# Performance work log

Measured on AMD Instinct MI355X. Metric: run time of the kernel, lower is better.

The kernel has to match this reference:

```python
import jax, jax.numpy as jnp
import numpy as np

HID = 128
EMB = 100

def _sru(x, W, b):
    # x: [B,L,D]; W: [D,3H]; b: [2H]. SRU (Lei et al.):
    #   u = [x_tilde, f_pre, r_pre]; c_t = f_t*c_{t-1} + (1-f_t)*x_tilde; h_t = r_t*tanh(c_t)
    u = jnp.einsum('bld,dk->blk', x, W)            # [B,L,3H]
    xt, fp, rp = jnp.split(u, 3, axis=-1)
    bf, br = jnp.split(b, 2)
    f = jax.nn.sigmoid(fp + bf)
    r = jax.nn.sigmoid(rp + br)
    g = (1.0 - f) * xt
    def comb(e1, e2):
        a1, b1 = e1
        a2, b2 = e2
        return a1 * a2, a2 * b1 + b2
    _, c = jax.lax.associative_scan(comb, (f, g), axis=1)  # parallel linear scan
    h = r * jnp.tanh(c)                             # [B,L,H]
    return h, c[:, -1]

def _conv_relu_gmax(x, w, bias, pad):
    # x: [B,256,1,1]; w: [16,256,k,k]; global max pool (interprets MaxPool2d(max_len) as global)
    y = jax.lax.conv_general_dilated(x, w, (1, 1), [(pad, pad), (pad, pad)],
                                     dimension_numbers=('NCHW', 'OIHW', 'NCHW'))
    y = jax.nn.relu(y + bias[None, :, None, None])
    return jnp.max(y, axis=(2, 3))                  # [B,16]

def setup_inputs() -> dict:
    key = jax.random.key(0)
    ks = jax.random.split(key, 12)
    B, L, V, NC = 8, 20000, 50000, 10
    index = jax.random.randint(ks[0], (B, L), 0, V, dtype=jnp.int64)
    emb = jax.random.normal(ks[1], (V, EMB), jnp.float32) * 0.1
    sru_W = jax.random.normal(ks[2], (EMB, 3 * HID), jnp.float32) / np.sqrt(EMB)
    sru_b = jnp.zeros((2 * HID,), jnp.float32)
    w1 = jax.random.normal(ks[3], (16, 2 * HID, 5, 5), jnp.float32) / np.sqrt(2 * HID * 25)
    b1 = jnp.zeros((16,), jnp.float32)
    w2 = jax.random.normal(ks[4], (16, 2 * HID, 4, 4), jnp.float32) / np.sqrt(2 * HID * 16)
    b2 = jnp.zeros((16,), jnp.float32)
    w3 = jax.random.normal(ks[5], (16, 2 * HID, 3, 3), jnp.float32) / np.sqrt(2 * HID * 9)
    b3 = jnp.zeros((16,), jnp.float32)
    out_W = jax.random.normal(ks[6], (48, NC), jnp.float32) / np.sqrt(48)
    out_b = jnp.zeros((NC,), jnp.float32)
    return {"index": index, "emb": emb, "sru_W": sru_W, "sru_b": sru_b,
            "w1": w1, "b1": b1, "w2": w2, "b2": b2, "w3": w3, "b3": b3,
            "out_W": out_W, "out_b": out_b}

def reference(index, emb, sru_W, sru_b, w1, b1, w2, b2, w3, b3, out_W, out_b):
    B, L = index.shape
    # Faithful reproduction of the aliased in-place reversal: y = index, then
    # y[row][j] = index[L-1-j] mutates the shared buffer, yielding
    # mutated[j] = orig[L-1-j] for j <= (L-1)//2 else orig[j]; BOTH branches
    # then embed this same mutated tensor (x aliases index in the original).
    j = jnp.arange(L)
    mutated = jnp.where((2 * j)[None, :] <= (L - 1), index[:, L - 1 - j], index)
    x = emb[mutated]                                # [B,L,100]
    h, _ = _sru(x, sru_W, sru_b)                    # both SRU passes see identical input
    hcat = jnp.concatenate([h, h], axis=2)          # [B,L,256]
    pooled = jnp.mean(hcat, axis=1)                 # AvgPool1d(kernel=L) -> [B,256]
    xc = pooled[:, :, None, None]                   # [B,256,1,1]
    f1 = _conv_relu_gmax(xc, w1, b1, 2)
    f2 = _conv_relu_gmax(xc, w2, b2, 2)
    f3 = _conv_relu_gmax(xc, w3, b3, 2)
    feats = jnp.concatenate([f1, f2, f3], axis=1)   # [B,48]
    return feats @ out_W + out_b                    # 'pred' logits [B,n_class]
```

## Files before the change

kernel.cpp:

```cpp
#include <hip/hip_runtime.h>
#include <math.h>

#define EMBD 100
#define HIDN 128
#define LSEQ 20000
#define TCS  128
#define WUP  32
#define NCH  ((LSEQ + TCS - 1) / TCS)

typedef __attribute__((ext_vector_type(8))) short bf16x8;
typedef __attribute__((ext_vector_type(4))) float f32x4;
typedef unsigned int u32;

__device__ __forceinline__ u32 f2bf_rne(float x) {
    u32 u = __float_as_uint(x);
    return (u + 0x7FFFu + ((u >> 16) & 1u)) >> 16;
}
__device__ __forceinline__ float bf2f(u32 b) { return __uint_as_float(b << 16); }

__device__ __forceinline__ float sigmoid_fast(float x) {
    float e = __expf(-x);
    return __builtin_amdgcn_rcpf(1.f + e);
}
__device__ __forceinline__ float tanh_fast(float x) {
    float e = __expf(2.f * x);
    return 1.f - 2.f * __builtin_amdgcn_rcpf(e + 1.f);
}

__global__ __launch_bounds__(256) void k_prep(const float* __restrict__ W,
                                              short* __restrict__ Wpk,
                                              const float* __restrict__ w1,
                                              const float* __restrict__ w2,
                                              const float* __restrict__ w3,
                                              float* __restrict__ Wc)
{
    const int blk = blockIdx.x;
    if (blk < 192) {
        int t = blk * 256 + threadIdx.x;
        int k = t / 384, c = t - k * 384;
        float w = (k < EMBD) ? W[k * 384 + c] : 0.0f;
        int kt = k >> 5, ct = c >> 4;
        int cg = ct & 7, c3 = ct >> 3;
        int l  = ((k >> 3) & 3) * 16 + (c & 15);
        int j  = k & 7;
        Wpk[(size_t)cg * 6144 + kt * 1536 + c3 * 512 + l * 8 + j] = (short)f2bf_rne(w);
    } else {
        int t = (blk - 192) * 256 + threadIdx.x;
        if (t >= 14 * 16 * HIDN) return;
        int k = t & 127, d = t >> 7;
        int o = d & 15, tap = d >> 4;
        const float* w; int KH, ki, kj;
        if (tap == 0)      { w = w1; KH = 5; ki = 2; kj = 2; }
        else if (tap < 5)  { w = w2; KH = 4; int p = tap - 1; ki = 1 + (p >> 1); kj = 1 + (p & 1); }
        else               { w = w3; KH = 3; int p = tap - 5; ki = p / 3; kj = p % 3; }
        float v = w[((size_t)(o * 256 + k) * KH + ki) * KH + kj]
                + w[((size_t)(o * 256 + k + 128) * KH + ki) * KH + kj];
        Wc[(size_t)d * HIDN + k] = v;
    }
}

__global__ __launch_bounds__(256) void k_build(const float* __restrict__ emb,
                                               const short* __restrict__ Wpk,
                                               const float* __restrict__ bias,
                                               u32* __restrict__ FGR, int V)
{
    const int lane = threadIdx.x & 63;
    const int wave = threadIdx.x >> 6;
    const int v0   = blockIdx.x * 128 + wave * 32;
    const int arow = lane & 15;
    const int kgrp = lane >> 4;

    bf16x8 Ah[2][4];
#pragma unroll
    for (int s = 0; s < 2; s++) {
        int va = v0 + s * 16 + arow; if (va > V - 1) va = V - 1;
        const float* erow = emb + (size_t)va * EMBD;
#pragma unroll
        for (int kt = 0; kt < 4; kt++) {
            int kbase = kt * 32 + kgrp * 8;
#pragma unroll
            for (int j = 0; j < 8; j++) {
                int k = kbase + j;
                Ah[s][kt][j] = (short)((k < EMBD) ? f2bf_rne(erow[k]) : 0);
            }
        }
    }

#pragma unroll 1
    for (int cgp = 0; cgp < 4; cgp++) {
        f32x4 acc[2][2][3];
#pragma unroll
        for (int s = 0; s < 2; s++)
#pragma unroll
            for (int h = 0; h < 2; h++)
#pragma unroll
                for (int c3 = 0; c3 < 3; c3++)
                    acc[s][h][c3] = f32x4{0.f, 0.f, 0.f, 0.f};

#pragma unroll
        for (int kt = 0; kt < 4; kt++) {
            const short* pL = Wpk + (size_t)cgp * 6144 + kt * 1536 + lane * 8;
            const short* pH = pL + 4 * 6144;
#pragma unroll
            for (int c3 = 0; c3 < 3; c3++) {
                bf16x8 BL = *reinterpret_cast<const bf16x8*>(pL + c3 * 512);
                bf16x8 BH = *reinterpret_cast<const bf16x8*>(pH + c3 * 512);
#pragma unroll
                for (int s = 0; s < 2; s++) {
                    acc[s][0][c3] = __builtin_amdgcn_mfma_f32_16x16x32_bf16(Ah[s][kt], BL, acc[s][0][c3], 0, 0, 0);
                    acc[s][1][c3] = __builtin_amdgcn_mfma_f32_16x16x32_bf16(Ah[s][kt], BH, acc[s][1][c3], 0, 0, 0);
                }
            }
        }

        const int kl = cgp * 16 + arow;
        const float bfL = bias[kl],      brL = bias[128 + kl];
        const float bfH = bias[kl + 64], brH = bias[192 + kl];
#pragma unroll
        for (int s = 0; s < 2; s++) {
#pragma unroll
            for (int reg = 0; reg < 4; reg++) {
                int v = v0 + s * 16 + kgrp * 4 + reg;
                if (v < V) {
                    float fL = sigmoid_fast(acc[s][0][1][reg] + bfL);
                    float rL = sigmoid_fast(acc[s][0][2][reg] + brL);
                    float gL = (1.f - fL) * acc[s][0][0][reg];
                    float fH = sigmoid_fast(acc[s][1][1][reg] + bfH);
                    float rH = sigmoid_fast(acc[s][1][2][reg] + brH);
                    float gH = (1.f - fH) * acc[s][1][0][reg];
                    u32 d0 = f2bf_rne(fL) | (f2bf_rne(gL) << 16);
                    u32 d1 = f2bf_rne(fH) | (f2bf_rne(gH) << 16);
                    u32 d2 = f2bf_rne(rL) | (f2bf_rne(rH) << 16);
                    *reinterpret_cast<uint2*>(FGR + (size_t)v * 192 + kl * 2) = make_uint2(d0, d1);
                    FGR[(size_t)v * 192 + 128 + kl] = d2;
                }
            }
        }
    }
}

__device__ __forceinline__ int mut_src(int t) {
    return (2 * t <= LSEQ - 1) ? (LSEQ - 1 - t) : t;
}

#define LOADB(Abuf, Rbuf, BT, NEEDR)                                       \
    { const int* sp = svp + (BT) * 8;                                      \
      _Pragma("unroll")                                                    \
      for (int i = 0; i < 8; i++) {                                        \
          int v = sp[i];                                                   \
          Abuf[i] = fgp[(size_t)v * 96 + lane];                            \
          Rbuf[i] = (NEEDR) ? FGR[(size_t)v * 192 + 128 + lane] : 0u;      \
      } }

#define STEP8(Abuf, Rbuf, DO_H)                                            \
    _Pragma("unroll")                                                      \
    for (int i = 0; i < 8; i++) {                                          \
        uint2 w = Abuf[i];                                                 \
        c0 = fmaf(__uint_as_float(w.x << 16), c0, __uint_as_float(w.x & 0xFFFF0000u)); \
        c1 = fmaf(__uint_as_float(w.y << 16), c1, __uint_as_float(w.y & 0xFFFF0000u)); \
        if (DO_H) {                                                        \
            u32 rr = Rbuf[i];                                              \
            h0 = fmaf(__uint_as_float(rr << 16),         tanh_fast(c0), h0); \
            h1 = fmaf(__uint_as_float(rr & 0xFFFF0000u), tanh_fast(c1), h1); \
        } }

__global__ __launch_bounds__(256) void k_scan(const int* __restrict__ idx,
                                              const u32* __restrict__ FGR,
                                              float* __restrict__ hpart)
{
    const int wave = threadIdx.x >> 6, lane = threadIdx.x & 63;
    const int ch = blockIdx.x * 4 + wave, b = blockIdx.y;
    if (ch >= NCH) return;
    const int t0 = ch * TCS;
    const int tw = (t0 >= WUP) ? (t0 - WUP) : 0;
    const int tend = (t0 + TCS < LSEQ) ? (t0 + TCS) : LSEQ;
    const int nsteps = tend - tw;
    const int nb = nsteps >> 3;
    const int wb = (t0 - tw) >> 3;
    __shared__ int sv[4][TCS + WUP];
    int* svp = sv[wave];
    for (int s = lane; s < nsteps; s += 64)
        svp[s] = idx[b * LSEQ + mut_src(tw + s)];

    const uint2* fgp = reinterpret_cast<const uint2*>(FGR);
    float c0 = 0.f, c1 = 0.f, h0 = 0.f, h1 = 0.f;
    uint2 A0[8], A1[8], A2[8]; u32 R0[8], R1[8], R2[8];

    LOADB(A0, R0, 0, 0 >= wb);
    LOADB(A1, R1, 1, 1 >= wb);

    for (int bt = 0; bt < nb; bt++) {
        if (bt + 2 < nb) { LOADB(A2, R2, bt + 2, bt + 2 >= wb); }
        if (bt >= wb) { STEP8(A0, R0, true); }
        else          { STEP8(A0, R0, false); }
#pragma unroll
        for (int i = 0; i < 8; i++) {
            A0[i] = A1[i]; R0[i] = R1[i];
            A1[i] = A2[i]; R1[i] = R2[i];
        }
    }

    float* hp = hpart + (size_t)(b * NCH + ch) * HIDN;
    hp[lane]      = h0;
    hp[lane + 64] = h1;
}

__global__ __launch_bounds__(1024) void k_head(const float* __restrict__ hpart,
                                               const float* __restrict__ Wc,
                                               const float* __restrict__ b1,
                                               const float* __restrict__ b2,
                                               const float* __restrict__ b3,
                                               const float* __restrict__ oW,
                                               const float* __restrict__ ob,
                                               float* __restrict__ out)
{
    __shared__ float red[8][HIDN];
    __shared__ float m[HIDN];
    __shared__ float dots[224];
    __shared__ float feats[48];
    const int b = blockIdx.x, tid = threadIdx.x;

    {
        int k = tid & 127, g = tid >> 7;
        float s = 0.f;
        for (int ch = g; ch < NCH; ch += 8)
            s += hpart[(size_t)(b * NCH + ch) * HIDN + k];
        red[g][k] = s;
    }
    __syncthreads();
    if (tid < HIDN) {
        float s = 0.f;
#pragma unroll
        for (int g = 0; g < 8; g++) s += red[g][tid];
        m[tid] = s * (1.0f / (float)LSEQ);
    }
    __syncthreads();

    if (tid < 896) {
        int q = tid & 3, d = tid >> 2;
        const float4* wp = reinterpret_cast<const float4*>(Wc + (size_t)d * HIDN + q * 32);
        const float4* mp = reinterpret_cast<const float4*>(m + q * 32);
        float s = 0.f;
#pragma unroll
        for (int j = 0; j < 8; j++) {
            float4 w4 = wp[j];
            float4 m4 = mp[j];
            s = fmaf(w4.x, m4.x, s);
            s = fmaf(w4.y, m4.y, s);
            s = fmaf(w4.z, m4.z, s);
            s = fmaf(w4.w, m4.w, s);
        }
        s += __shfl_xor(s, 1);
        s += __shfl_xor(s, 2);
        if (q == 0) dots[d] = s;
    }
    __syncthreads();

    if (tid < 16) {
        float f1 = fmaxf(dots[tid] + b1[tid], 0.f);
        float v2 = dots[16 + tid];
        for (int p = 2; p <= 4; p++) v2 = fmaxf(v2, dots[p * 16 + tid]);
        float f2 = fmaxf(v2 + b2[tid], 0.f);
        float v3 = dots[5 * 16 + tid];
        for (int p = 6; p <= 13; p++) v3 = fmaxf(v3, dots[p * 16 + tid]);
        float f3 = fmaxf(v3 + b3[tid], 0.f);
        feats[tid] = f1; feats[16 + tid] = f2; feats[32 + tid] = f3;
    }
    __syncthreads();

    if (tid < 10) {
        float s = ob[tid];
#pragma unroll
        for (int j = 0; j < 48; j++) s = fmaf(feats[j], oW[j * 10 + tid], s);
        out[b * 10 + tid] = s;
    }
}

extern "C" void kernel_launch(void* const* d_in, const int* in_sizes, int n_in,
                              void* d_out, int out_size, void* d_ws, size_t ws_size,
                              hipStream_t stream)
{
    const int*   index = (const int*)  d_in[0];
    const float* emb   = (const float*)d_in[1];
    const float* sru_W = (const float*)d_in[2];
    const float* sru_b = (const float*)d_in[3];
    const float* w1    = (const float*)d_in[4];
    const float* b1    = (const float*)d_in[5];
    const float* w2    = (const float*)d_in[6];
    const float* b2    = (const float*)d_in[7];
    const float* w3    = (const float*)d_in[8];
    const float* b3    = (const float*)d_in[9];
    const float* oW    = (const float*)d_in[10];
    const float* ob    = (const float*)d_in[11];
    float* out = (float*)d_out;

    const int V = in_sizes[1] / EMBD;
    const int B = in_sizes[0] / LSEQ;

    char* ws = (char*)d_ws;
    size_t off = 0;
    auto alloc = [&](size_t bytes) -> void* {
        void* p = ws + off;
        off += (bytes + 255) & ~(size_t)255;
        return p;
    };
    u32*   FGR = (u32*)alloc((size_t)V * 192 * sizeof(u32));
    float* hp  = (float*)alloc((size_t)B * NCH * HIDN * sizeof(float));
    short* Wpk = (short*)alloc((size_t)8 * 6144 * sizeof(short));
    float* Wc  = (float*)alloc((size_t)14 * 16 * HIDN * sizeof(float));
    (void)ws_size; (void)n_in; (void)out_size;

    hipLaunchKernelGGL(k_prep, dim3(192 + 112), dim3(256), 0, stream,
                       sru_W, Wpk, w1, w2, w3, Wc);
    hipLaunchKernelGGL(k_build, dim3((V + 127) / 128), dim3(256), 0, stream,
                       emb, Wpk, sru_b, FGR, V);
    hipLaunchKernelGGL(k_scan, dim3((NCH + 3) / 4, B), dim3(256), 0, stream,
                       index, FGR, hp);
    hipLaunchKernelGGL(k_head, dim3(B), dim3(1024), 0, stream,
                       hp, Wc, b1, b2, b3, oW, ob, out);
}
```

Before: 69.60 us.

## Stage packed SRU weights in double-buffered LDS in build kernel; halve scan warmup

The vocabulary projection kernel now copies each column group's packed bf16 weights into shared memory once per block, double-buffering the next group while the current one is used, and the four waves read B fragments from LDS rather than each re-reading them from global memory. This adds barriers and 48KB of LDS per block, which may lower occupancy. Separately, the chunked scan warmup length is halved, which cuts redundant recurrence work per chunk but shortens the decay window used to approximate the carried-in state.

```diff
diff --git a/kernel.cpp b/kernel.cpp
--- a/kernel.cpp
+++ b/kernel.cpp
@@ -5,7 +5,7 @@
 #define HIDN 128
 #define LSEQ 20000
 #define TCS  128
-#define WUP  32
+#define WUP  16
 #define NCH  ((LSEQ + TCS - 1) / TCS)
 
 typedef __attribute__((ext_vector_type(8))) short bf16x8;
@@ -64,8 +64,10 @@
                                                const float* __restrict__ bias,
                                                u32* __restrict__ FGR, int V)
 {
-    const int lane = threadIdx.x & 63;
-    const int wave = threadIdx.x >> 6;
+    __shared__ __align__(16) short sW[2][12288];
+    const int tid  = threadIdx.x;
+    const int lane = tid & 63;
+    const int wave = tid >> 6;
     const int v0   = blockIdx.x * 128 + wave * 32;
     const int arow = lane & 15;
     const int kgrp = lane >> 4;
@@ -86,8 +88,29 @@
         }
     }
 
+    const uint4* wsrc = reinterpret_cast<const uint4*>(Wpk);
+    {
+        uint4* dst = reinterpret_cast<uint4*>(sW[0]);
+#pragma unroll
+        for (int i = tid; i < 768; i += 256) {
+            dst[i]       = wsrc[i];
+            dst[768 + i] = wsrc[4 * 768 + i];
+        }
+    }
+    __syncthreads();
+
 #pragma unroll 1
     for (int cgp = 0; cgp < 4; cgp++) {
+        const int cur = cgp & 1;
+        if (cgp + 1 < 4) {
+            uint4* dst = reinterpret_cast<uint4*>(sW[cur ^ 1]);
+#pragma unroll
+            for (int i = tid; i < 768; i += 256) {
+                dst[i]       = wsrc[(cgp + 1) * 768 + i];
+                dst[768 + i] = wsrc[(cgp + 5) * 768 + i];
+            }
+        }
+
         f32x4 acc[2][2][3];
 #pragma unroll
         for (int s = 0; s < 2; s++)
@@ -99,8 +122,8 @@
 
 #pragma unroll
         for (int kt = 0; kt < 4; kt++) {
-            const short* pL = Wpk + (size_t)cgp * 6144 + kt * 1536 + lane * 8;
-            const short* pH = pL + 4 * 6144;
+            const short* pL = &sW[cur][kt * 1536 + lane * 8];
+            const short* pH = pL + 6144;
 #pragma unroll
             for (int c3 = 0; c3 < 3; c3++) {
                 bf16x8 BL = *reinterpret_cast<const bf16x8*>(pL + c3 * 512);
@@ -136,6 +159,7 @@
                 }
             }
         }
+        __syncthreads();
     }
 }
 
```

After: 63.15 us. 1.1x faster.
